# Kernel tuning notes

Hardware: AMD Instinct MI355X
Metric: run time of the kernel (lower is better)

The kernel has to match this reference:

```python
import jax, jax.numpy as jnp
import numpy as np

EMB = 128
HEAD = 8
QKV = 16
SQRT_EMB = 11.313708498984761
CLIP = 10.0
B, P, N = 64, 100, 1000


def setup_inputs() -> dict:
    key = jax.random.key(0)
    ks = jax.random.split(key, 12)
    encoded_last_node = jax.random.normal(ks[0], (B, P, EMB), jnp.float32)
    load = jax.random.uniform(ks[1], (B, P), jnp.float32)
    time = jax.random.uniform(ks[2], (B, P), jnp.float32)
    cur_dist = jax.random.uniform(ks[3], (B, P, N), jnp.float32)
    mask_bits = jax.random.uniform(ks[4], (B, P, N)) < 0.1
    ninf_mask = jnp.where(mask_bits, -1e9, 0.0).astype(jnp.float32)
    noise = jax.random.uniform(ks[5], (B, P, N), jnp.float32)
    encoded_nodes = jax.random.normal(ks[6], (B, N, EMB), jnp.float32)
    s = 1.0 / np.sqrt(EMB)
    Wq = jax.random.uniform(ks[7], (EMB + 2, HEAD * QKV), jnp.float32, -s, s)
    Wk = jax.random.uniform(ks[8], (EMB, HEAD * QKV), jnp.float32, -s, s)
    Wv = jax.random.uniform(ks[9], (EMB, HEAD * QKV), jnp.float32, -s, s)
    Wc = jax.random.uniform(ks[10], (HEAD * QKV, EMB), jnp.float32, -s, s)
    bc = jax.random.uniform(ks[11], (EMB,), jnp.float32, -s, s)
    return {"encoded_last_node": encoded_last_node, "load": load, "time": time,
            "cur_dist": cur_dist, "ninf_mask": ninf_mask, "noise": noise,
            "encoded_nodes": encoded_nodes, "Wq": Wq, "Wk": Wk, "Wv": Wv,
            "Wc": Wc, "bc": bc}


def _heads(x):
    # (B, n, H*D) -> (B, H, n, D)
    b, n, _ = x.shape
    return x.reshape(b, n, HEAD, QKV).transpose(0, 2, 1, 3)


def reference(encoded_last_node, load, time, cur_dist, ninf_mask, noise,
              encoded_nodes, Wq, Wk, Wv, Wc, bc):
    # set_kv
    k = _heads(encoded_nodes @ Wk)   # (B,H,N,D)
    v = _heads(encoded_nodes @ Wv)   # (B,H,N,D)

    # query from last node + load + time
    input_cat = jnp.concatenate(
        [encoded_last_node, load[:, :, None], time[:, :, None]], axis=2)
    q = _heads(input_cat @ Wq)       # (B,H,P,D)

    # multi-head attention with rank3 ninf mask
    score = jnp.einsum('bhpd,bhnd->bhpn', q, k) / jnp.sqrt(
        jnp.asarray(QKV, jnp.float32))
    score = score + ninf_mask[:, None, :, :]
    weights = jax.nn.softmax(score, axis=3)
    out = jnp.einsum('bhpn,bhnd->bhpd', weights, v)
    out_concat = out.transpose(0, 2, 1, 3).reshape(B, P, HEAD * QKV)
    mh_atten_out = out_concat @ Wc + bc            # (B,P,EMB)

    # single-head pointer logits
    score2 = jnp.einsum('bpe,bne->bpn', mh_atten_out, encoded_nodes)
    score_scaled = score2 / SQRT_EMB

    # heuristic / noise blend
    st_cost = cur_dist + cur_dist
    raw_heuristic = -jnp.log(st_cost + 1e-6)
    a = 1.0 / (1.0 + 2.0 ** ((100.0 - N) / 50.0))
    b = 1.0 - a
    mixed_signal = a * raw_heuristic + b * noise
    s = score_scaled + mixed_signal
    score_clipped = CLIP * jnp.tanh(s)
    score_masked = score_clipped + ninf_mask
    probs = jax.nn.softmax(score_masked, axis=2)
    return probs
```

## Files before the change

### kernel.cpp

```cpp
#include <hip/hip_runtime.h>
#include <hip/hip_bf16.h>

#define B_   64
#define P_   100
#define N_   1000
#define EMB_ 128
#define HEAD_ 8
#define QKV_ 16
#define QT   4

constexpr double kTwoPowNeg18 = 3.814697265625e-06;
constexpr double kA_d = 1.0 / (1.0 + kTwoPowNeg18);

__global__ __launch_bounds__(256) void kv_proj(
    const float* __restrict__ en, const float* __restrict__ Wk,
    const float* __restrict__ Wv, float* __restrict__ K2, float* __restrict__ V2)
{
    __shared__ __align__(16) float e_s[32][128];
    const int t = threadIdx.x;
    const int j = t & 127;
    const int half = t >> 7;
    const int r0 = blockIdx.x * 32;

    {
        const float4* src = (const float4*)(en + (size_t)r0 * 128);
        float4* dst = (float4*)&e_s[0][0];
        #pragma unroll
        for (int k = 0; k < 4; ++k) dst[t + 256 * k] = src[t + 256 * k];
    }
    __syncthreads();

    float ak[16], av[16];
    #pragma unroll
    for (int r = 0; r < 16; ++r) { ak[r] = 0.f; av[r] = 0.f; }

    const int rb = half * 16;
    for (int i4 = 0; i4 < 32; ++i4) {
        float wk4[4], wv4[4];
        #pragma unroll
        for (int c = 0; c < 4; ++c) {
            wk4[c] = Wk[(4 * i4 + c) * 128 + j];
            wv4[c] = Wv[(4 * i4 + c) * 128 + j];
        }
        #pragma unroll
        for (int r = 0; r < 16; ++r) {
            const float4 e4 = *(const float4*)&e_s[rb + r][4 * i4];
            ak[r] = fmaf(e4.x, wk4[0], fmaf(e4.y, wk4[1],
                    fmaf(e4.z, wk4[2], fmaf(e4.w, wk4[3], ak[r]))));
            av[r] = fmaf(e4.x, wv4[0], fmaf(e4.y, wv4[1],
                    fmaf(e4.z, wv4[2], fmaf(e4.w, wv4[3], av[r]))));
        }
    }

    const int h = j >> 4, d = j & 15;
    #pragma unroll
    for (int r = 0; r < 16; ++r) {
        const int row = r0 + rb + r;
        const int bb = row / N_;
        const int n = row - bb * N_;
        const size_t idx = ((size_t)(bb * HEAD_ + h) * N_ + n) * 16 + d;
        K2[idx] = ak[r];
        V2[idx] = av[r];
    }
}

__global__ __launch_bounds__(128) void q_proj(
    const float* __restrict__ eln, const float* __restrict__ load_,
    const float* __restrict__ time_, const float* __restrict__ Wq,
    float* __restrict__ Q)
{
    __shared__ __align__(16) float e_s[8][132];
    const int j  = threadIdx.x;
    const int r0 = blockIdx.x * 8;

    #pragma unroll
    for (int r = 0; r < 8; ++r) {
        const int row = r0 + r;
        e_s[r][j] = eln[(size_t)row * 128 + j];
        if (j == 0) {
            e_s[r][128] = load_[row];
            e_s[r][129] = time_[row];
        }
    }
    __syncthreads();

    float a[8];
    #pragma unroll
    for (int r = 0; r < 8; ++r) a[r] = 0.f;

    for (int i4 = 0; i4 < 32; ++i4) {
        float w4[4];
        #pragma unroll
        for (int c = 0; c < 4; ++c) w4[c] = Wq[(4 * i4 + c) * 128 + j];
        #pragma unroll
        for (int r = 0; r < 8; ++r) {
            const float4 e4 = *(const float4*)&e_s[r][4 * i4];
            a[r] = fmaf(e4.x, w4[0], fmaf(e4.y, w4[1],
                   fmaf(e4.z, w4[2], fmaf(e4.w, w4[3], a[r]))));
        }
    }
    #pragma unroll
    for (int i = 128; i < 130; ++i) {
        const float w = Wq[i * 128 + j];
        #pragma unroll
        for (int r = 0; r < 8; ++r)
            a[r] = fmaf(e_s[r][i], w, a[r]);
    }

    #pragma unroll
    for (int r = 0; r < 8; ++r)
        Q[(size_t)(r0 + r) * 128 + j] = a[r];
}

__global__ __launch_bounds__(256) void attn_heads(
    const float* __restrict__ K2, const float* __restrict__ V2,
    const float* __restrict__ Q, const float* __restrict__ ninf,
    float* __restrict__ out_g)
{
    __shared__ __align__(16) float sc[QT][1008];
    __shared__ __align__(16) float q_s[QT][16];
    __shared__ __align__(16) float part_s[4][QT][16];
    __shared__ float invden_s[QT];

    const int blk = blockIdx.x;
    const int h   = blk & 7;
    const int j9  = blk >> 3;
    const int pt  = j9 % 25;
    const int b   = j9 / 25;
    const int bp0 = b * P_ + pt * QT;
    const int t    = threadIdx.x;
    const int lane = t & 63;
    const int wv   = t >> 6;

    if (t < 64) q_s[t >> 4][t & 15] =
        Q[(size_t)(bp0 + (t >> 4)) * 128 + h * 16 + (t & 15)];
    __syncthreads();

    float qr[QT][16];
    #pragma unroll
    for (int q = 0; q < QT; ++q)
        #pragma unroll
        for (int c = 0; c < 4; ++c)
            *(float4*)&qr[q][4 * c] = *(const float4*)&q_s[q][4 * c];

    const float* nf0 = ninf + (size_t)bp0 * N_;
    float msk[QT][4];
    #pragma unroll
    for (int i = 0; i < 4; ++i) {
        const int n = t + 256 * i;
        if (n < N_) {
            #pragma unroll
            for (int q = 0; q < QT; ++q) msk[q][i] = nf0[q * N_ + n];
        }
    }

    const float* Kh = K2 + (size_t)(b * HEAD_ + h) * N_ * 16;
    #pragma unroll
    for (int i = 0; i < 4; ++i) {
        const int n = t + 256 * i;
        if (n < N_) {
            const float4* kr = (const float4*)(Kh + (size_t)n * 16);
            const float4 k0 = kr[0], k1 = kr[1], k2 = kr[2], k3 = kr[3];
            #pragma unroll
            for (int q = 0; q < QT; ++q) {
                float d = k0.x * qr[q][0]  + k0.y * qr[q][1]
                        + k0.z * qr[q][2]  + k0.w * qr[q][3]
                        + k1.x * qr[q][4]  + k1.y * qr[q][5]
                        + k1.z * qr[q][6]  + k1.w * qr[q][7]
                        + k2.x * qr[q][8]  + k2.y * qr[q][9]
                        + k2.z * qr[q][10] + k2.w * qr[q][11]
                        + k3.x * qr[q][12] + k3.y * qr[q][13]
                        + k3.z * qr[q][14] + k3.w * qr[q][15];
                sc[q][n] = d * 0.25f + msk[q][i];
            }
        }
    }
    __syncthreads();

    {
        const int q = wv;
        float m = -INFINITY;
        for (int n = lane; n < N_; n += 64) m = fmaxf(m, sc[q][n]);
        #pragma unroll
        for (int off = 32; off > 0; off >>= 1) m = fmaxf(m, __shfl_xor(m, off));
        float s = 0.f;
        for (int n = lane; n < N_; n += 64) {
            const float e = __expf(sc[q][n] - m);
            sc[q][n] = e;
            s += e;
        }
        #pragma unroll
        for (int off = 32; off > 0; off >>= 1) s += __shfl_xor(s, off);
        if (lane == 0) invden_s[q] = 1.f / s;
    }
    __syncthreads();

    {
        const int c = lane & 3, g = lane >> 2;
        const float* Vh = V2 + (size_t)(b * HEAD_ + h) * N_ * 16 + 4 * c;
        const int n0 = wv * 250;
        float4 a0 = {0.f, 0.f, 0.f, 0.f}, a1 = a0, a2 = a0, a3 = a0;
        #pragma unroll 4
        for (int i = 0; i < 16; ++i) {
            const int nn = 16 * i + g;
            if (nn < 250) {
                const int n = n0 + nn;
                const float4 v4 = *(const float4*)(Vh + (size_t)n * 16);
                const float w0 = sc[0][n], w1 = sc[1][n];
                const float w2 = sc[2][n], w3 = sc[3][n];
                a0.x = fmaf(w0, v4.x, a0.x); a0.y = fmaf(w0, v4.y, a0.y);
                a0.z = fmaf(w0, v4.z, a0.z); a0.w = fmaf(w0, v4.w, a0.w);
                a1.x = fmaf(w1, v4.x, a1.x); a1.y = fmaf(w1, v4.y, a1.y);
                a1.z = fmaf(w1, v4.z, a1.z); a1.w = fmaf(w1, v4.w, a1.w);
                a2.x = fmaf(w2, v4.x, a2.x); a2.y = fmaf(w2, v4.y, a2.y);
                a2.z = fmaf(w2, v4.z, a2.z); a2.w = fmaf(w2, v4.w, a2.w);
                a3.x = fmaf(w3, v4.x, a3.x); a3.y = fmaf(w3, v4.y, a3.y);
                a3.z = fmaf(w3, v4.z, a3.z); a3.w = fmaf(w3, v4.w, a3.w);
            }
        }
        #pragma unroll
        for (int off = 4; off <= 32; off <<= 1) {
            a0.x += __shfl_xor(a0.x, off); a0.y += __shfl_xor(a0.y, off);
            a0.z += __shfl_xor(a0.z, off); a0.w += __shfl_xor(a0.w, off);
            a1.x += __shfl_xor(a1.x, off); a1.y += __shfl_xor(a1.y, off);
            a1.z += __shfl_xor(a1.z, off); a1.w += __shfl_xor(a1.w, off);
            a2.x += __shfl_xor(a2.x, off); a2.y += __shfl_xor(a2.y, off);
            a2.z += __shfl_xor(a2.z, off); a2.w += __shfl_xor(a2.w, off);
            a3.x += __shfl_xor(a3.x, off); a3.y += __shfl_xor(a3.y, off);
            a3.z += __shfl_xor(a3.z, off); a3.w += __shfl_xor(a3.w, off);
        }
        if (g == 0) {
            *(float4*)&part_s[wv][0][4 * c] = a0;
            *(float4*)&part_s[wv][1][4 * c] = a1;
            *(float4*)&part_s[wv][2][4 * c] = a2;
            *(float4*)&part_s[wv][3][4 * c] = a3;
        }
    }
    __syncthreads();

    if (t < 64) {
        const int q = t >> 4, d = t & 15;
        const float s = part_s[0][q][d] + part_s[1][q][d]
                      + part_s[2][q][d] + part_s[3][q][d];
        out_g[(size_t)(bp0 + q) * 128 + h * 16 + d] = s * invden_s[q];
    }
}

__global__ __launch_bounds__(256) void ptr_epilogue(
    const float* __restrict__ out_g, const float* __restrict__ en,
    const float* __restrict__ Wc, const float* __restrict__ bc,
    const float* __restrict__ cur_dist, const float* __restrict__ ninf,
    const float* __restrict__ noise, float* __restrict__ probs)
{
    __shared__ __align__(16) float sc[QT][1008];
    __shared__ __align__(16) float out_s[QT][128];
    __shared__ __align__(16) float mh_s[QT][128];

    const int blk  = blockIdx.x;
    const int rX   = blk & 7;
    const int j9   = blk >> 3;
    const int pt   = j9 % 25;
    const int b    = (j9 / 25) * 8 + rX;
    const int bp0  = b * P_ + pt * QT;
    const int t    = threadIdx.x;
    const int lane = t & 63;
    const int wv   = t >> 6;

    if (t < 128)
        ((float4*)&out_s[0][0])[t] = ((const float4*)(out_g + (size_t)bp0 * 128))[t];
    __syncthreads();

    {
        const int e = t & 127, qh = t >> 7;
        float a0 = bc[e], a1 = a0;
        for (int i = 0; i < 128; ++i) {
            const float w = Wc[i * 128 + e];
            a0 = fmaf(out_s[qh][i], w, a0);
            a1 = fmaf(out_s[qh + 2][i], w, a1);
        }
        mh_s[qh][e] = a0;
        mh_s[qh + 2][e] = a1;
    }
    __syncthreads();

    {
        const int k16 = lane & 15, g = lane >> 4;
        float4 mh0[QT], mh1[QT];
        #pragma unroll
        for (int q = 0; q < QT; ++q) {
            mh0[q] = *(const float4*)&mh_s[q][k16 * 8];
            mh1[q] = *(const float4*)&mh_s[q][k16 * 8 + 4];
        }
        const float* enb = en + (size_t)b * N_ * 128;
        for (int nb = 4 * wv; nb < N_; nb += 16) {
            const int n = nb + g;
            const float4* er = (const float4*)(enb + (size_t)n * 128 + k16 * 8);
            const float4 e0 = er[0], e1 = er[1];
            float acc[QT];
            #pragma unroll
            for (int q = 0; q < QT; ++q) {
                acc[q] = e0.x * mh0[q].x + e0.y * mh0[q].y
                       + e0.z * mh0[q].z + e0.w * mh0[q].w
                       + e1.x * mh1[q].x + e1.y * mh1[q].y
                       + e1.z * mh1[q].z + e1.w * mh1[q].w;
            }
            #pragma unroll
            for (int q = 0; q < QT; ++q) {
                float v = acc[q];
                v += __shfl_xor(v, 1);
                v += __shfl_xor(v, 2);
                v += __shfl_xor(v, 4);
                v += __shfl_xor(v, 8);
                if (k16 == 0) sc[q][n] = v;
            }
        }
    }
    __syncthreads();

    {
        const int q  = wv;
        const int bp = bp0 + q;
        const float* cd = cur_dist + (size_t)bp * N_;
        const float* nz = noise    + (size_t)bp * N_;
        const float* nf = ninf     + (size_t)bp * N_;
        const float A   = (float)kA_d;
        const float Bc2 = (float)(1.0 - kA_d);

        float m = -INFINITY;
        for (int n = lane; n < N_; n += 64) {
            const float s2 = sc[q][n] / 11.3137085f;
            const float st = cd[n] + cd[n];
            const float rh = -logf(st + 1e-6f);
            const float s  = s2 + A * rh + Bc2 * nz[n];
            const float sm = 10.f * tanhf(s) + nf[n];
            sc[q][n] = sm;
            m = fmaxf(m, sm);
        }
        #pragma unroll
        for (int off = 32; off > 0; off >>= 1) m = fmaxf(m, __shfl_xor(m, off));

        float s = 0.f;
        for (int n = lane; n < N_; n += 64) {
            const float e = __expf(sc[q][n] - m);
            sc[q][n] = e;
            s += e;
        }
        #pragma unroll
        for (int off = 32; off > 0; off >>= 1) s += __shfl_xor(s, off);

        const float inv = 1.f / s;
        float* out = probs + (size_t)bp * N_;
        for (int n = lane; n < N_; n += 64) out[n] = sc[q][n] * inv;
    }
}

extern "C" void kernel_launch(void* const* d_in, const int* in_sizes, int n_in,
                              void* d_out, int out_size, void* d_ws, size_t ws_size,
                              hipStream_t stream)
{
    const float* eln      = (const float*)d_in[0];
    const float* load_    = (const float*)d_in[1];
    const float* time_    = (const float*)d_in[2];
    const float* cur_dist = (const float*)d_in[3];
    const float* ninf     = (const float*)d_in[4];
    const float* noise    = (const float*)d_in[5];
    const float* en       = (const float*)d_in[6];
    const float* Wq       = (const float*)d_in[7];
    const float* Wk       = (const float*)d_in[8];
    const float* Wv       = (const float*)d_in[9];
    const float* Wc       = (const float*)d_in[10];
    const float* bc       = (const float*)d_in[11];
    float* probs = (float*)d_out;

    float* K2    = (float*)d_ws;
    float* V2    = K2 + (size_t)B_ * HEAD_ * N_ * 16;
    float* Q     = V2 + (size_t)B_ * HEAD_ * N_ * 16;
    float* out_g = Q  + (size_t)B_ * P_ * 128;

    kv_proj<<<(B_ * N_) / 32, 256, 0, stream>>>(en, Wk, Wv, K2, V2);
    q_proj<<<(B_ * P_) / 8, 128, 0, stream>>>(eln, load_, time_, Wq, Q);
    attn_heads<<<B_ * HEAD_ * (P_ / QT), 256, 0, stream>>>(K2, V2, Q, ninf, out_g);
    ptr_epilogue<<<(B_ * P_) / QT, 256, 0, stream>>>(out_g, en, Wc, bc,
                                                     cur_dist, ninf, noise, probs);
}
```

Measured before the change: 495.6 us.

## Register-block kv_proj over two output columns and pin pointer-logit operands

kv_proj now gives each thread 16 rows times two output columns (j and j+64) for both K and V, and each block covers 64 rows instead of 32. This doubles reuse of each shared-memory row load and halves the block count. In the pointer epilogue, empty asm constraints keep the mh vectors in registers, and the n-loop is unrolled by two to raise memory-level parallelism. The cost is higher register pressure (64 accumulators per thread), which may lower occupancy.

```diff
diff --git a/kernel.cpp b/kernel.cpp
--- a/kernel.cpp
+++ b/kernel.cpp
@@ -12,55 +12,66 @@
 constexpr double kTwoPowNeg18 = 3.814697265625e-06;
 constexpr double kA_d = 1.0 / (1.0 + kTwoPowNeg18);
 
+#define KEEP4(v) asm volatile("" : "+v"((v).x), "+v"((v).y), "+v"((v).z), "+v"((v).w))
+
 __global__ __launch_bounds__(256) void kv_proj(
     const float* __restrict__ en, const float* __restrict__ Wk,
     const float* __restrict__ Wv, float* __restrict__ K2, float* __restrict__ V2)
 {
-    __shared__ __align__(16) float e_s[32][128];
-    const int t = threadIdx.x;
-    const int j = t & 127;
-    const int half = t >> 7;
-    const int r0 = blockIdx.x * 32;
+    __shared__ __align__(16) float e_s[64][128];
+    const int t  = threadIdx.x;
+    const int j  = t & 63;
+    const int rb = (t >> 6) * 16;
+    const int r0 = blockIdx.x * 64;
 
     {
         const float4* src = (const float4*)(en + (size_t)r0 * 128);
         float4* dst = (float4*)&e_s[0][0];
         #pragma unroll
-        for (int k = 0; k < 4; ++k) dst[t + 256 * k] = src[t + 256 * k];
-    }
-    __syncthreads();
-
-    float ak[16], av[16];
-    #pragma unroll
-    for (int r = 0; r < 16; ++r) { ak[r] = 0.f; av[r] = 0.f; }
-
-    const int rb = half * 16;
+        for (int k = 0; k < 8; ++k) dst[t + 256 * k] = src[t + 256 * k];
+    }
+    __syncthreads();
+
+    float ak0[16], ak1[16], av0[16], av1[16];
+    #pragma unroll
+    for (int r = 0; r < 16; ++r) { ak0[r] = 0.f; ak1[r] = 0.f; av0[r] = 0.f; av1[r] = 0.f; }
+
     for (int i4 = 0; i4 < 32; ++i4) {
-        float wk4[4], wv4[4];
+        float wk0[4], wk1[4], wv0[4], wv1[4];
         #pragma unroll
         for (int c = 0; c < 4; ++c) {
-            wk4[c] = Wk[(4 * i4 + c) * 128 + j];
-            wv4[c] = Wv[(4 * i4 + c) * 128 + j];
+            const int rowi = (4 * i4 + c) * 128;
+            wk0[c] = Wk[rowi + j];
+            wk1[c] = Wk[rowi + j + 64];
+            wv0[c] = Wv[rowi + j];
+            wv1[c] = Wv[rowi + j + 64];
         }
         #pragma unroll
         for (int r = 0; r < 16; ++r) {
             const float4 e4 = *(const float4*)&e_s[rb + r][4 * i4];
-            ak[r] = fmaf(e4.x, wk4[0], fmaf(e4.y, wk4[1],
-                    fmaf(e4.z, wk4[2], fmaf(e4.w, wk4[3], ak[r]))));
-            av[r] = fmaf(e4.x, wv4[0], fmaf(e4.y, wv4[1],
-                    fmaf(e4.z, wv4[2], fmaf(e4.w, wv4[3], av[r]))));
-        }
-    }
-
-    const int h = j >> 4, d = j & 15;
+            ak0[r] = fmaf(e4.x, wk0[0], fmaf(e4.y, wk0[1],
+                     fmaf(e4.z, wk0[2], fmaf(e4.w, wk0[3], ak0[r]))));
+            ak1[r] = fmaf(e4.x, wk1[0], fmaf(e4.y, wk1[1],
+                     fmaf(e4.z, wk1[2], fmaf(e4.w, wk1[3], ak1[r]))));
+            av0[r] = fmaf(e4.x, wv0[0], fmaf(e4.y, wv0[1],
+                     fmaf(e4.z, wv0[2], fmaf(e4.w, wv0[3], av0[r]))));
+            av1[r] = fmaf(e4.x, wv1[0], fmaf(e4.y, wv1[1],
+                     fmaf(e4.z, wv1[2], fmaf(e4.w, wv1[3], av1[r]))));
+        }
+    }
+
+    const int h0 = j >> 4, d0 = j & 15;
+    const int h1 = (j + 64) >> 4, d1 = j & 15;
     #pragma unroll
     for (int r = 0; r < 16; ++r) {
         const int row = r0 + rb + r;
         const int bb = row / N_;
         const int n = row - bb * N_;
-        const size_t idx = ((size_t)(bb * HEAD_ + h) * N_ + n) * 16 + d;
-        K2[idx] = ak[r];
-        V2[idx] = av[r];
+        const size_t base = ((size_t)bb * HEAD_ * N_ + n) * 16;
+        K2[base + (size_t)h0 * N_ * 16 + d0] = ak0[r];
+        K2[base + (size_t)h1 * N_ * 16 + d1] = ak1[r];
+        V2[base + (size_t)h0 * N_ * 16 + d0] = av0[r];
+        V2[base + (size_t)h1 * N_ * 16 + d1] = av1[r];
     }
 }
 
@@ -290,8 +301,11 @@
         for (int q = 0; q < QT; ++q) {
             mh0[q] = *(const float4*)&mh_s[q][k16 * 8];
             mh1[q] = *(const float4*)&mh_s[q][k16 * 8 + 4];
+            KEEP4(mh0[q]);
+            KEEP4(mh1[q]);
         }
         const float* enb = en + (size_t)b * N_ * 128;
+        #pragma unroll 2
         for (int nb = 4 * wv; nb < N_; nb += 16) {
             const int n = nb + g;
             const float4* er = (const float4*)(enb + (size_t)n * 128 + k16 * 8);
@@ -377,7 +391,7 @@
     float* Q     = V2 + (size_t)B_ * HEAD_ * N_ * 16;
     float* out_g = Q  + (size_t)B_ * P_ * 128;
 
-    kv_proj<<<(B_ * N_) / 32, 256, 0, stream>>>(en, Wk, Wv, K2, V2);
+    kv_proj<<<(B_ * N_) / 64, 256, 0, stream>>>(en, Wk, Wv, K2, V2);
     q_proj<<<(B_ * P_) / 8, 128, 0, stream>>>(eln, load_, time_, Wq, Q);
     attn_heads<<<B_ * HEAD_ * (P_ / QT), 256, 0, stream>>>(K2, V2, Q, ninf, out_g);
     ptr_epilogue<<<(B_ * P_) / QT, 256, 0, stream>>>(out_g, en, Wc, bc,
```

New measurement: 488.2 us. Within noise of the previous version (-1.5%).
